# Performance work log

Measured on AMD Instinct MI355X. Metric: run time of the kernel, lower is better.

The kernel has to match this reference:

```python
import jax, jax.numpy as jnp
import numpy as np

N_NODES = 100000
N_EDGES = 1600000
N_GRAPHS = 128
D = 64
EPS = 1e-5


def layer_norm(h, gamma, beta):
    mu = jnp.mean(h, axis=-1, keepdims=True)
    var = jnp.var(h, axis=-1, keepdims=True)
    return (h - mu) * jax.lax.rsqrt(var + EPS) * gamma + beta


def setup_inputs() -> dict:
    key = jax.random.key(0)
    ks = jax.random.split(key, 9)
    x = jax.random.normal(ks[0], (N_NODES, D), dtype=jnp.float32)
    edge_index = jax.random.randint(ks[1], (2, N_EDGES), 0, N_NODES, dtype=jnp.int64)
    batch = jnp.sort(jax.random.randint(ks[2], (N_NODES,), 0, N_GRAPHS, dtype=jnp.int64))
    graph_embed = jax.random.normal(ks[3], (N_GRAPHS, D), dtype=jnp.float32)
    s = 1.0 / np.sqrt(D)
    W_self = jax.random.uniform(ks[4], (D, D), jnp.float32, -s, s)
    W_neigh = jax.random.uniform(ks[5], (D, D), jnp.float32, -s, s)
    b = jax.random.uniform(ks[6], (D,), jnp.float32, -s, s)
    gamma = jnp.ones((D,), jnp.float32)
    beta = jnp.zeros((D,), jnp.float32)
    return {"x": x, "edge_index": edge_index, "batch": batch,
            "graph_embed": graph_embed, "W_self": W_self, "W_neigh": W_neigh,
            "b": b, "gamma": gamma, "beta": beta}


def reference(x, edge_index, batch, graph_embed, W_self, W_neigh, b, gamma, beta):
    src, dst = edge_index[0], edge_index[1]
    # mean neighbor aggregation: gather src features, scatter-add into dst
    msg_sum = jax.ops.segment_sum(x[src], dst, num_segments=N_NODES)  # [N, D]
    deg = jax.ops.segment_sum(jnp.ones((N_EDGES,), x.dtype), dst, num_segments=N_NODES)
    h_neigh = msg_sum / jnp.maximum(deg, 1.0)[:, None]
    # SAGEConv combine
    node_out = x @ W_self + h_neigh @ W_neigh + b  # [N, D]
    # graph_aggr='add' pooling over batch assignment
    graph_out = jax.ops.segment_sum(node_out, batch, num_segments=N_GRAPHS)  # [G, D]
    # residual (channel_match=True -> no projection)
    node_out = node_out + x
    graph_out = graph_out + graph_embed
    # norm then act; note: original applies norm TWICE to graph_out and no ReLU on it
    node_out = jax.nn.relu(layer_norm(node_out, gamma, beta))
    graph_out = layer_norm(layer_norm(graph_out, gamma, beta), gamma, beta)
    return (node_out, graph_out)
```

## Files before the change

### kernel.cpp

```cpp
#include <hip/hip_runtime.h>

#define N_NODES  100000
#define N_EDGES  1600000
#define N_GRAPHS 128
#define DD       64
#define EPSV     1e-5f

#define BSH      5
#define BMASK    31
#define NBUCK    3125
#define CAPB     768

#define THRP     1024
#define EPT      16
#define BLKE     (THRP*EPT)
#define NBLK     ((N_EDGES + BLKE - 1) / BLKE)

#define O_CUR   0u
#define O_BKT   200704u
#define O_GACC  9801216u
#define O_XB    9834496u
#define O_WTF   22634496u
#define WS_NEED (O_WTF + 16384u)

typedef __attribute__((ext_vector_type(8))) short bf16x8;
typedef __attribute__((ext_vector_type(4))) float f32x4;

__device__ __forceinline__ ushort bf16rne(float f) {
  uint u = __float_as_uint(f);
  return (ushort)((u + 0x7FFFu + ((u >> 16) & 1u)) >> 16);
}
__device__ __forceinline__ uint pk2(float lo, float hi) {
  return (uint)bf16rne(lo) | ((uint)bf16rne(hi) << 16);
}

__global__ __launch_bounds__(256) void cast_k(const float* __restrict__ x, ushort* __restrict__ xb,
                                              int* __restrict__ cur, float* __restrict__ gacc) {
  int i = blockIdx.x * 256 + threadIdx.x;
  if (i < NBUCK * 16) cur[i] = 0;
  if (i < N_GRAPHS * DD) gacc[i] = 0.f;
  float4 v = ((const float4*)x)[i];
  uint4 u = *(const uint4*)&v;
  ushort4 o;
  o.x = (ushort)((u.x + 0x7FFFu + ((u.x >> 16) & 1)) >> 16);
  o.y = (ushort)((u.y + 0x7FFFu + ((u.y >> 16) & 1)) >> 16);
  o.z = (ushort)((u.z + 0x7FFFu + ((u.z >> 16) & 1)) >> 16);
  o.w = (ushort)((u.w + 0x7FFFu + ((u.w >> 16) & 1)) >> 16);
  ((ushort4*)xb)[i] = o;
}

__global__ __launch_bounds__(1024) void scatP_k(const int* __restrict__ ei, int* __restrict__ cur,
                                                int* __restrict__ bkt,
                                                const float* __restrict__ Wself,
                                                const float* __restrict__ Wneigh,
                                                ushort* __restrict__ wtf) {
  __shared__ int hist[NBUCK];
  int t = threadIdx.x;
  if (blockIdx.x == 0) {
    int lane = t & 63, ks = (t >> 6) & 3, tile = (t >> 8) & 1, nt = t >> 9;
    int brow = (nt << 5) + (tile << 4) + (lane & 15);
    int k0 = (ks << 5) + (((lane >> 4) & 3) << 3);
    uint4 o;
    uint p[4];
#pragma unroll
    for (int jj = 0; jj < 4; ++jj) {
      int k = k0 + jj * 2;
      float w0 = (k < 64)     ? Wself[k * DD + brow]       : Wneigh[(k - 64) * DD + brow];
      float w1 = (k + 1 < 64) ? Wself[(k + 1) * DD + brow] : Wneigh[(k - 63) * DD + brow];
      p[jj] = pk2(w0, w1);
    }
    o.x = p[0]; o.y = p[1]; o.z = p[2]; o.w = p[3];
    ((uint4*)wtf)[t] = o;
  }
  for (int i = t; i < NBUCK; i += THRP) hist[i] = 0;
  __syncthreads();
  int e0 = blockIdx.x * BLKE;
  int pk[EPT], bn[EPT];
#pragma unroll
  for (int j = 0; j < EPT; ++j) {
    int e = e0 + j * THRP + t;
    bn[j] = -1;
    if (e < N_EDGES) {
      int s = ei[e], d = ei[N_EDGES + e];
      bn[j] = d >> BSH;
      pk[j] = s | ((d & BMASK) << 17);
      atomicAdd(&hist[bn[j]], 1);
    }
  }
  __syncthreads();
  for (int b = t; b < NBUCK; b += THRP) {
    int c = hist[b];
    hist[b] = c ? atomicAdd(&cur[b * 16], c) : 0;
  }
  __syncthreads();
#pragma unroll
  for (int j = 0; j < EPT; ++j) {
    if (bn[j] >= 0) {
      int sp = atomicAdd(&hist[bn[j]], 1);
      if (sp < CAPB) bkt[bn[j] * CAPB + sp] = pk[j];
    }
  }
}

__global__ __launch_bounds__(256, 8) void aggM_k(const ushort* __restrict__ xb,
                                                 const int* __restrict__ cur,
                                                 const int* __restrict__ bkt,
                                                 const ushort* __restrict__ wtf,
                                                 const float* __restrict__ bvec,
                                                 const float* __restrict__ gamma,
                                                 const float* __restrict__ beta,
                                                 const int* __restrict__ batch,
                                                 float* __restrict__ gacc,
                                                 float* __restrict__ out) {
  __shared__ short As[32 * 128];
  __shared__ float Cbuf[32 * 65];
  __shared__ int sorted[CAPB];
  __shared__ int hist[32], startc[32], curl[32];
  int t = threadIdx.x;
  int b = blockIdx.x;
  int node0 = b << BSH;
  if (t < 32) hist[t] = 0;
  {
    uint4 v = ((const uint4*)(xb + (size_t)node0 * DD))[t];
    uint r = (uint)t >> 3, c = (uint)t & 7;
    *(uint4*)((char*)As + r * 256u + ((c * 16u) ^ ((r & 7u) << 4))) = v;
  }
  __syncthreads();
  int n = cur[b * 16];
  if (n > CAPB) n = CAPB;
  int boff = b * CAPB;
  int w0 = -1, w1 = -1, w2 = -1;
  if (t < n)       { w0 = bkt[boff + t];       atomicAdd(&hist[w0 >> 17], 1); }
  if (t + 256 < n) { w1 = bkt[boff + t + 256]; atomicAdd(&hist[w1 >> 17], 1); }
  if (t + 512 < n) { w2 = bkt[boff + t + 512]; atomicAdd(&hist[w2 >> 17], 1); }
  __syncthreads();
  if (t < 32) startc[t] = hist[t];
  __syncthreads();
  for (int off = 1; off < 32; off <<= 1) {
    int v = 0;
    if (t < 32) { v = startc[t]; if (t >= off) v += startc[t - off]; }
    __syncthreads();
    if (t < 32) startc[t] = v;
    __syncthreads();
  }
  if (t < 32) { int ex = startc[t] - hist[t]; startc[t] = ex; curl[t] = ex; }
  __syncthreads();
  if (w0 >= 0) { int p = atomicAdd(&curl[w0 >> 17], 1); sorted[p] = w0 & 0x1FFFF; }
  if (w1 >= 0) { int p = atomicAdd(&curl[w1 >> 17], 1); sorted[p] = w1 & 0x1FFFF; }
  if (w2 >= 0) { int p = atomicAdd(&curl[w2 >> 17], 1); sorted[p] = w2 & 0x1FFFF; }
  __syncthreads();
  int wl   = __builtin_amdgcn_readfirstlane(t >> 6);
  int lane = t & 63;
  int g    = lane >> 4;
  int sub  = lane & 15;
  const uint2* xb2 = (const uint2*)xb;
  for (int r = wl; r < 32; r += 4) {
    int s0 = startc[r], dg = hist[r];
    int dgm1 = dg > 0 ? dg - 1 : 0;
    float a0 = 0.f, a1 = 0.f, a2 = 0.f, a3 = 0.f;
    for (int j = 0; j < dg; j += 16) {
      int e0 = j + g, e1 = j + 4 + g, e2 = j + 8 + g, e3 = j + 12 + g;
      int i0 = sorted[s0 + (e0 < dg ? e0 : dgm1)];
      int i1 = sorted[s0 + (e1 < dg ? e1 : dgm1)];
      int i2 = sorted[s0 + (e2 < dg ? e2 : dgm1)];
      int i3 = sorted[s0 + (e3 < dg ? e3 : dgm1)];
      uint2 u0 = xb2[(size_t)i0 * 16 + sub];
      uint2 u1 = xb2[(size_t)i1 * 16 + sub];
      uint2 u2 = xb2[(size_t)i2 * 16 + sub];
      uint2 u3 = xb2[(size_t)i3 * 16 + sub];
      if (e0 >= dg) { u0.x = 0u; u0.y = 0u; }
      if (e1 >= dg) { u1.x = 0u; u1.y = 0u; }
      if (e2 >= dg) { u2.x = 0u; u2.y = 0u; }
      if (e3 >= dg) { u3.x = 0u; u3.y = 0u; }
      a0 += (__uint_as_float(u0.x << 16) + __uint_as_float(u1.x << 16))
          + (__uint_as_float(u2.x << 16) + __uint_as_float(u3.x << 16));
      a1 += (__uint_as_float(u0.x & 0xFFFF0000u) + __uint_as_float(u1.x & 0xFFFF0000u))
          + (__uint_as_float(u2.x & 0xFFFF0000u) + __uint_as_float(u3.x & 0xFFFF0000u));
      a2 += (__uint_as_float(u0.y << 16) + __uint_as_float(u1.y << 16))
          + (__uint_as_float(u2.y << 16) + __uint_as_float(u3.y << 16));
      a3 += (__uint_as_float(u0.y & 0xFFFF0000u) + __uint_as_float(u1.y & 0xFFFF0000u))
          + (__uint_as_float(u2.y & 0xFFFF0000u) + __uint_as_float(u3.y & 0xFFFF0000u));
    }
#pragma unroll
    for (int off = 16; off <= 32; off <<= 1) {
      a0 += __shfl_xor(a0, off);
      a1 += __shfl_xor(a1, off);
      a2 += __shfl_xor(a2, off);
      a3 += __shfl_xor(a3, off);
    }
    if (g == 0) {
      float inv = 1.f / fmaxf((float)dg, 1.f);
      uint2 pw;
      pw.x = pk2(a0 * inv, a1 * inv);
      pw.y = pk2(a2 * inv, a3 * inv);
      uint rr = (uint)r;
      *(uint2*)((char*)As + rr * 256u + ((128u + (uint)sub * 8u) ^ ((rr & 7u) << 4))) = pw;
    }
  }
  __syncthreads();
  f32x4 acc0 = {0.f, 0.f, 0.f, 0.f}, acc1 = {0.f, 0.f, 0.f, 0.f};
  uint mrow  = (uint)(wl >> 1) << 4;
  int  nt    = wl & 1;
  uint arow  = mrow + (uint)(lane & 15);
  uint kc    = ((uint)(lane >> 4)) * 16u;
#pragma unroll 1
  for (int ks = 0; ks < 4; ++ks) {
    uint kb = (uint)ks * 64u + kc;
    bf16x8 af = *(const bf16x8*)((const char*)As + arow * 256u + (kb ^ ((arow & 7u) << 4)));
    bf16x8 b0 = *(const bf16x8*)(wtf + (size_t)(((nt * 2 + 0) * 4 + ks) * 64 + lane) * 8);
    bf16x8 b1 = *(const bf16x8*)(wtf + (size_t)(((nt * 2 + 1) * 4 + ks) * 64 + lane) * 8);
    acc0 = __builtin_amdgcn_mfma_f32_16x16x32_bf16(af, b0, acc0, 0, 0, 0);
    acc1 = __builtin_amdgcn_mfma_f32_16x16x32_bf16(af, b1, acc1, 0, 0, 0);
  }
  {
    uint nbase = (uint)nt << 5;
    uint rr = mrow + (((uint)(lane >> 4)) << 2);
    uint cc = nbase + (uint)(lane & 15);
#pragma unroll
    for (int j = 0; j < 4; ++j) {
      uint rj = rr + (uint)j;
      Cbuf[rj * 65u + cc]       = acc0[j];
      Cbuf[rj * 65u + cc + 16u] = acc1[j];
    }
  }
  __syncthreads();
  float bv  = bvec[lane];
  float gv  = gamma[lane];
  float btv = beta[lane];
  int r0 = wl * 8;
  int gprev = -1; float pool = 0.f;
#pragma unroll
  for (int m = 0; m < 8; ++m) {
    uint r = (uint)(r0 + m);
    int node = node0 + r0 + m;
    float cval = Cbuf[r * 65u + (uint)lane];
    float tmp = cval + bv;
    int gi = batch[node];
    if (gi != gprev) {
      if (gprev >= 0) atomicAdd(&gacc[gprev * DD + lane], pool);
      pool = 0.f; gprev = gi;
    }
    pool += tmp;
    ushort xv16 = *(const ushort*)((const char*)As + r * 256u + (((uint)lane * 2u) ^ ((r & 7u) << 4)));
    float val = tmp + __uint_as_float((uint)xv16 << 16);
    float s = val;
    for (int off = 32; off; off >>= 1) s += __shfl_xor(s, off);
    float mu  = s * (1.f / 64.f);
    float dlt = val - mu;
    float ss  = dlt * dlt;
    for (int off = 32; off; off >>= 1) ss += __shfl_xor(ss, off);
    float rstd = rsqrtf(ss * (1.f / 64.f) + EPSV);
    float o = dlt * rstd * gv + btv;
    out[(size_t)node * DD + lane] = fmaxf(o, 0.f);
  }
  if (gprev >= 0) atomicAdd(&gacc[gprev * DD + lane], pool);
}

__global__ __launch_bounds__(256) void graph_k(const float* __restrict__ gacc, const float* __restrict__ gemb,
                                               const float* __restrict__ gamma, const float* __restrict__ beta,
                                               float* __restrict__ out) {
  int lane = threadIdx.x & 63;
  int w = blockIdx.x * 4 + (threadIdx.x >> 6);
  if (w >= N_GRAPHS) return;
  float v = gacc[w * DD + lane] + gemb[w * DD + lane];
  float gv = gamma[lane], btv = beta[lane];
#pragma unroll
  for (int it = 0; it < 2; ++it) {
    float s = v;
    for (int off = 32; off; off >>= 1) s += __shfl_xor(s, off);
    float mu  = s * (1.f / 64.f);
    float d   = v - mu;
    float ss  = d * d;
    for (int off = 32; off; off >>= 1) ss += __shfl_xor(ss, off);
    v = d * rsqrtf(ss * (1.f / 64.f) + EPSV) * gv + btv;
  }
  out[(size_t)N_NODES * DD + w * DD + lane] = v;
}

extern "C" void kernel_launch(void* const* d_in, const int* in_sizes, int n_in,
                              void* d_out, int out_size, void* d_ws, size_t ws_size,
                              hipStream_t stream) {
  const float* x      = (const float*)d_in[0];
  const int*   ei     = (const int*)d_in[1];
  const int*   batch  = (const int*)d_in[2];
  const float* gemb   = (const float*)d_in[3];
  const float* Wself  = (const float*)d_in[4];
  const float* Wneigh = (const float*)d_in[5];
  const float* bvec   = (const float*)d_in[6];
  const float* gamma  = (const float*)d_in[7];
  const float* beta   = (const float*)d_in[8];

  char* ws = (char*)d_ws;
  int*    cur  = (int*)(ws + O_CUR);
  int*    bkt  = (int*)(ws + O_BKT);
  float*  gacc = (float*)(ws + O_GACC);
  ushort* xb   = (ushort*)(ws + O_XB);
  ushort* wtf  = (ushort*)(ws + O_WTF);
  float*  outf = (float*)d_out;

  cast_k <<<N_NODES * DD / 4 / 256, 256, 0, stream>>>(x, xb, cur, gacc);
  scatP_k<<<NBLK, THRP, 0, stream>>>(ei, cur, bkt, Wself, Wneigh, wtf);
  aggM_k <<<NBUCK, 256, 0, stream>>>(xb, cur, bkt, wtf, bvec, gamma, beta,
                                     batch, gacc, outf);
  graph_k<<<N_GRAPHS / 4, 256, 0, stream>>>(gacc, gemb, gamma, beta, outf);
}
```

Baseline: 95.34 us.

## Use wave-shuffle scan, prescaled byte offsets, zero-row gather and packed float2 adds

Replaces the multi-barrier shared-memory prefix scan over 32 bucket counts with a single-wave shuffle-up scan. Stores neighbor indices pre-multiplied to byte offsets (plus 512) so out-of-range slots gather a zero row from a zeroed region of the workspace instead of clamping and masking after the load. Accumulates through float2 vector adds so the compiler can emit packed FP32 instructions. This trims barriers and per-edge ALU work in the gather loop, but relies on the 512 bytes before xb (the tail of gacc) being zeroed and on extra padding in the sorted array.

```diff
diff --git a/kernel.cpp b/kernel.cpp
--- a/kernel.cpp
+++ b/kernel.cpp
@@ -25,6 +25,7 @@
 
 typedef __attribute__((ext_vector_type(8))) short bf16x8;
 typedef __attribute__((ext_vector_type(4))) float f32x4;
+typedef __attribute__((ext_vector_type(2))) float f32x2;
 
 __device__ __forceinline__ ushort bf16rne(float f) {
   uint u = __float_as_uint(f);
@@ -39,6 +40,7 @@
   int i = blockIdx.x * 256 + threadIdx.x;
   if (i < NBUCK * 16) cur[i] = 0;
   if (i < N_GRAPHS * DD) gacc[i] = 0.f;
+  if (i < 128) gacc[N_GRAPHS * DD + i] = 0.f;
   float4 v = ((const float4*)x)[i];
   uint4 u = *(const uint4*)&v;
   ushort4 o;
@@ -114,7 +116,7 @@
                                                  float* __restrict__ out) {
   __shared__ short As[32 * 128];
   __shared__ float Cbuf[32 * 65];
-  __shared__ int sorted[CAPB];
+  __shared__ int sorted[CAPB + 16];
   __shared__ int hist[32], startc[32], curl[32];
   int t = threadIdx.x;
   int b = blockIdx.x;
@@ -134,53 +136,54 @@
   if (t + 256 < n) { w1 = bkt[boff + t + 256]; atomicAdd(&hist[w1 >> 17], 1); }
   if (t + 512 < n) { w2 = bkt[boff + t + 512]; atomicAdd(&hist[w2 >> 17], 1); }
   __syncthreads();
-  if (t < 32) startc[t] = hist[t];
-  __syncthreads();
-  for (int off = 1; off < 32; off <<= 1) {
-    int v = 0;
-    if (t < 32) { v = startc[t]; if (t >= off) v += startc[t - off]; }
-    __syncthreads();
-    if (t < 32) startc[t] = v;
-    __syncthreads();
-  }
-  if (t < 32) { int ex = startc[t] - hist[t]; startc[t] = ex; curl[t] = ex; }
-  __syncthreads();
-  if (w0 >= 0) { int p = atomicAdd(&curl[w0 >> 17], 1); sorted[p] = w0 & 0x1FFFF; }
-  if (w1 >= 0) { int p = atomicAdd(&curl[w1 >> 17], 1); sorted[p] = w1 & 0x1FFFF; }
-  if (w2 >= 0) { int p = atomicAdd(&curl[w2 >> 17], 1); sorted[p] = w2 & 0x1FFFF; }
+  if (t < 32) {
+    int h = hist[t];
+    int v = h;
+#pragma unroll
+    for (int off = 1; off < 32; off <<= 1) {
+      int u = __shfl_up(v, off);
+      if (t >= off) v += u;
+    }
+    startc[t] = v - h;
+    curl[t]   = v - h;
+  }
+  __syncthreads();
+  if (w0 >= 0) { int p = atomicAdd(&curl[w0 >> 17], 1); sorted[p] = ((w0 & 0x1FFFF) << 7) + 512; }
+  if (w1 >= 0) { int p = atomicAdd(&curl[w1 >> 17], 1); sorted[p] = ((w1 & 0x1FFFF) << 7) + 512; }
+  if (w2 >= 0) { int p = atomicAdd(&curl[w2 >> 17], 1); sorted[p] = ((w2 & 0x1FFFF) << 7) + 512; }
   __syncthreads();
   int wl   = __builtin_amdgcn_readfirstlane(t >> 6);
   int lane = t & 63;
   int g    = lane >> 4;
   int sub  = lane & 15;
-  const uint2* xb2 = (const uint2*)xb;
+  const char* zb = (const char*)xb - 512;
+  uint subb = (uint)sub * 8u;
   for (int r = wl; r < 32; r += 4) {
     int s0 = startc[r], dg = hist[r];
-    int dgm1 = dg > 0 ? dg - 1 : 0;
-    float a0 = 0.f, a1 = 0.f, a2 = 0.f, a3 = 0.f;
+    f32x2 A01 = {0.f, 0.f}, A23 = {0.f, 0.f};
     for (int j = 0; j < dg; j += 16) {
       int e0 = j + g, e1 = j + 4 + g, e2 = j + 8 + g, e3 = j + 12 + g;
-      int i0 = sorted[s0 + (e0 < dg ? e0 : dgm1)];
-      int i1 = sorted[s0 + (e1 < dg ? e1 : dgm1)];
-      int i2 = sorted[s0 + (e2 < dg ? e2 : dgm1)];
-      int i3 = sorted[s0 + (e3 < dg ? e3 : dgm1)];
-      uint2 u0 = xb2[(size_t)i0 * 16 + sub];
-      uint2 u1 = xb2[(size_t)i1 * 16 + sub];
-      uint2 u2 = xb2[(size_t)i2 * 16 + sub];
-      uint2 u3 = xb2[(size_t)i3 * 16 + sub];
-      if (e0 >= dg) { u0.x = 0u; u0.y = 0u; }
-      if (e1 >= dg) { u1.x = 0u; u1.y = 0u; }
-      if (e2 >= dg) { u2.x = 0u; u2.y = 0u; }
-      if (e3 >= dg) { u3.x = 0u; u3.y = 0u; }
-      a0 += (__uint_as_float(u0.x << 16) + __uint_as_float(u1.x << 16))
-          + (__uint_as_float(u2.x << 16) + __uint_as_float(u3.x << 16));
-      a1 += (__uint_as_float(u0.x & 0xFFFF0000u) + __uint_as_float(u1.x & 0xFFFF0000u))
-          + (__uint_as_float(u2.x & 0xFFFF0000u) + __uint_as_float(u3.x & 0xFFFF0000u));
-      a2 += (__uint_as_float(u0.y << 16) + __uint_as_float(u1.y << 16))
-          + (__uint_as_float(u2.y << 16) + __uint_as_float(u3.y << 16));
-      a3 += (__uint_as_float(u0.y & 0xFFFF0000u) + __uint_as_float(u1.y & 0xFFFF0000u))
-          + (__uint_as_float(u2.y & 0xFFFF0000u) + __uint_as_float(u3.y & 0xFFFF0000u));
-    }
+      uint o0 = (uint)sorted[s0 + e0]; if (e0 >= dg) o0 = 0u;
+      uint o1 = (uint)sorted[s0 + e1]; if (e1 >= dg) o1 = 0u;
+      uint o2 = (uint)sorted[s0 + e2]; if (e2 >= dg) o2 = 0u;
+      uint o3 = (uint)sorted[s0 + e3]; if (e3 >= dg) o3 = 0u;
+      uint2 u0 = *(const uint2*)(zb + o0 + subb);
+      uint2 u1 = *(const uint2*)(zb + o1 + subb);
+      uint2 u2 = *(const uint2*)(zb + o2 + subb);
+      uint2 u3 = *(const uint2*)(zb + o3 + subb);
+      f32x2 v0, v1, v2, v3, y0, y1, y2, y3;
+      v0.x = __uint_as_float(u0.x << 16); v0.y = __uint_as_float(u0.x & 0xFFFF0000u);
+      v1.x = __uint_as_float(u1.x << 16); v1.y = __uint_as_float(u1.x & 0xFFFF0000u);
+      v2.x = __uint_as_float(u2.x << 16); v2.y = __uint_as_float(u2.x & 0xFFFF0000u);
+      v3.x = __uint_as_float(u3.x << 16); v3.y = __uint_as_float(u3.x & 0xFFFF0000u);
+      y0.x = __uint_as_float(u0.y << 16); y0.y = __uint_as_float(u0.y & 0xFFFF0000u);
+      y1.x = __uint_as_float(u1.y << 16); y1.y = __uint_as_float(u1.y & 0xFFFF0000u);
+      y2.x = __uint_as_float(u2.y << 16); y2.y = __uint_as_float(u2.y & 0xFFFF0000u);
+      y3.x = __uint_as_float(u3.y << 16); y3.y = __uint_as_float(u3.y & 0xFFFF0000u);
+      A01 += (v0 + v1) + (v2 + v3);
+      A23 += (y0 + y1) + (y2 + y3);
+    }
+    float a0 = A01.x, a1 = A01.y, a2 = A23.x, a3 = A23.y;
 #pragma unroll
     for (int off = 16; off <= 32; off <<= 1) {
       a0 += __shfl_xor(a0, off);
```

Result: faster. 92.82 us (-2.6%).
